# Kernel tuning notes

Hardware: AMD Instinct MI355X
Metric: run time of the kernel (lower is better)

The kernel has to match this reference:

```python
import jax, jax.numpy as jnp
import numpy as np

BITS = 4
MAXQ = (1 << BITS) - 1  # 15
PACK_BITS = 32
GROUP_SIZE = 128


def setup_inputs() -> dict:
    key = jax.random.key(0)
    k1, k2, k3, k4, k5 = jax.random.split(key, 5)
    in_f, out_f, tokens = 4096, 11008, 8192
    pack_factor = PACK_BITS // BITS  # 8
    n_groups = in_f // GROUP_SIZE  # 32
    x = jax.random.normal(k1, (tokens, in_f), dtype=jnp.float32)
    qweight = jax.random.randint(k2, (in_f // pack_factor, out_f), 0, 2147483647, dtype=jnp.int32)
    qzeros = jax.random.randint(k3, (n_groups, out_f // pack_factor), 0, 2147483647, dtype=jnp.int32)
    scales = jax.random.uniform(k4, (n_groups, out_f), dtype=jnp.float32) * 0.01 + 1e-3
    bias = jax.random.normal(k5, (out_f,), dtype=jnp.float32)
    g_idx = (jnp.arange(in_f, dtype=jnp.int32) // GROUP_SIZE).astype(jnp.int32)
    return {"x": x, "qweight": qweight, "qzeros": qzeros, "scales": scales, "bias": bias, "g_idx": g_idx}


def _dequantize(qweight, qzeros, scales, g_idx, in_features):
    # wf = [0, 4, 8, ..., 28]
    shifts = jnp.arange(0, PACK_BITS, BITS, dtype=jnp.int32)
    # unpack zeros: [G, out/8] -> [G, out/8, 8] -> [G, out]
    zeros = (qzeros[:, :, None] >> shifts[None, None, :]) & MAXQ
    zeros = zeros.reshape(scales.shape)
    # unpack weight: [in/8, out] -> [in/8, 8, out] -> [in, out]
    w = (qweight[:, None, :] >> shifts[None, :, None]) & MAXQ
    w = w.reshape(-1, scales.shape[1])[:in_features]
    # dequant: scales[g_idx] * (w - zeros[g_idx])
    return scales[g_idx] * (w - zeros[g_idx]).astype(scales.dtype)


def reference(x, qweight, qzeros, scales, bias, g_idx):
    W = _dequantize(qweight, qzeros, scales, g_idx, x.shape[1])  # [in, out]
    return x @ W + bias
```

## Files before the change

kernel.cpp:

```cpp
#include <hip/hip_runtime.h>
#include <hip/hip_bf16.h>

typedef __attribute__((ext_vector_type(8))) short short8;
typedef __attribute__((ext_vector_type(4))) float f32x4;
typedef __attribute__((ext_vector_type(4))) unsigned int uint4v;

#define BM 256
#define BN 256
#define BK 64

__device__ __forceinline__ void gl_lds16(const __hip_bfloat16* g, __hip_bfloat16* l) {
  __builtin_amdgcn_global_load_lds((const __attribute__((address_space(1))) void*)g,
                                   (__attribute__((address_space(3))) void*)l,
                                   16, 0, 0);
}

__global__ void prep_kernel(const int* __restrict__ qweight,
                            const int* __restrict__ qzeros,
                            const float* __restrict__ scales,
                            __hip_bfloat16* __restrict__ wp,
                            const float* __restrict__ x,
                            __hip_bfloat16* __restrict__ xp,
                            int N, int K, int M, int nDeq) {
  __shared__ __hip_bfloat16 tile[64 * 64];
  const int id = blockIdx.x;
  if (id < nDeq) {
    const int nb = N >> 8;
    const int n = (id % nb) * 256 + threadIdx.x;
    const int kc = id / nb;
    const int g = kc >> 4;
    const float s = scales[(size_t)g * N + n];
    const int zq = qzeros[(size_t)g * (N >> 3) + (n >> 3)];
    const float c = s * (float)((zq >> ((n & 7) * 4)) & 15);
    const int q = qweight[(size_t)kc * N + n];
    __hip_bfloat16 v[8];
#pragma unroll
    for (int j = 0; j < 8; j++)
      v[j] = __float2bfloat16(fmaf(s, (float)((q >> (4 * j)) & 15), -c));
    ((uint4v*)wp)[(size_t)kc * N + n] = *(const uint4v*)v;
  } else {
    const int id2 = id - nDeq;
    const int mb = M >> 6;
    const int m0 = (id2 % mb) * 64, k0 = (id2 / mb) * 64;
    const int t = threadIdx.x;
    const int mr = t >> 2, cq = t & 3;
    const float4* src = (const float4*)(x + (size_t)(m0 + mr) * K + k0 + cq * 16);
    const float4 a = src[0], b = src[1], c = src[2], d = src[3];
    __hip_bfloat16 v[16];
    v[0] = __float2bfloat16(a.x);  v[1] = __float2bfloat16(a.y);
    v[2] = __float2bfloat16(a.z);  v[3] = __float2bfloat16(a.w);
    v[4] = __float2bfloat16(b.x);  v[5] = __float2bfloat16(b.y);
    v[6] = __float2bfloat16(b.z);  v[7] = __float2bfloat16(b.w);
    v[8] = __float2bfloat16(c.x);  v[9] = __float2bfloat16(c.y);
    v[10] = __float2bfloat16(c.z); v[11] = __float2bfloat16(c.w);
    v[12] = __float2bfloat16(d.x); v[13] = __float2bfloat16(d.y);
    v[14] = __float2bfloat16(d.z); v[15] = __float2bfloat16(d.w);
    *(uint4v*)&tile[((cq * 2 + 0) * 64 + mr) * 8] = *(const uint4v*)&v[0];
    *(uint4v*)&tile[((cq * 2 + 1) * 64 + mr) * 8] = *(const uint4v*)&v[8];
    __syncthreads();
#pragma unroll
    for (int j = 0; j < 2; j++) {
      const int s = j * 256 + t;
      const int c8 = s >> 6, m = s & 63;
      ((uint4v*)xp)[(size_t)((k0 >> 3) + c8) * M + m0 + m] = *(const uint4v*)&tile[s * 8];
    }
  }
}

__global__ __launch_bounds__(512, 2) void gemm_kernel(
    const __hip_bfloat16* __restrict__ Xp,
    const __hip_bfloat16* __restrict__ Wp,
    const float* __restrict__ bias,
    float* __restrict__ C, int M, int N, int K) {
  __shared__ __hip_bfloat16 As[2][8 * 256 * 8];
  __shared__ __hip_bfloat16 Bs[2][8 * 256 * 8];
  const int tid = threadIdx.x;
  const int m0 = blockIdx.x * BM;
  const int n0 = blockIdx.y * BN;
  const int wid = tid >> 6, ln = tid & 63;
  const int wmoff = (wid >> 2) * 128;
  const int wnoff = (wid & 3) * 64;
  const int lr = ln & 15, q4 = ln >> 4;

  f32x4 acc[8][4] = {};
  const int NT = K >> 6;

  auto stageA = [&](int t, int hs, int buf) {
#pragma unroll
    for (int i = 0; i < 2; ++i) {
      const int s = i * 512 + tid;
      const int c8 = (hs << 2) + (s >> 8);
      const int row = s & 255;
      gl_lds16(Xp + ((size_t)(t * 8 + c8) * M + m0 + row) * 8,
               &As[buf][(c8 * 256 + row) * 8]);
    }
  };
  auto stageB = [&](int t, int hs, int buf) {
#pragma unroll
    for (int i = 0; i < 2; ++i) {
      const int s = i * 512 + tid;
      const int c8 = (hs << 2) + (s >> 8);
      const int row = s & 255;
      gl_lds16(Wp + ((size_t)(t * 8 + c8) * N + n0 + row) * 8,
               &Bs[buf][(c8 * 256 + row) * 8]);
    }
  };

  stageA(0, 0, 0); stageA(0, 1, 0); stageB(0, 0, 0); stageB(0, 1, 0);
  if (NT > 1) {
    stageA(1, 0, 1); stageB(1, 0, 1); stageA(1, 1, 1);
    asm volatile("s_waitcnt vmcnt(6)" ::: "memory");
  } else {
    asm volatile("s_waitcnt vmcnt(0)" ::: "memory");
  }
  __builtin_amdgcn_s_barrier();

  short8 a[2][4], b0[2][2], b1[2][2];

  for (int t = 0; t < NT; ++t) {
    const int cur = t & 1, nxt = cur ^ 1;
    const __hip_bfloat16* Ac = As[cur];
    const __hip_bfloat16* Bc = Bs[cur];

#pragma unroll
    for (int ks = 0; ks < 2; ++ks) {
#pragma unroll
      for (int mf = 0; mf < 4; ++mf)
        a[ks][mf] = *(const short8*)&Ac[((ks * 4 + q4) * 256 + wmoff + mf * 16 + lr) * 8];
#pragma unroll
      for (int nf = 0; nf < 2; ++nf)
        b0[ks][nf] = *(const short8*)&Bc[((ks * 4 + q4) * 256 + wnoff + nf * 16 + lr) * 8];
    }
    if (t + 1 < NT) stageB(t + 1, 1, nxt);
    __builtin_amdgcn_s_barrier();
    asm volatile("s_waitcnt lgkmcnt(0)" ::: "memory");
    __builtin_amdgcn_s_setprio(1);
#pragma unroll
    for (int mf = 0; mf < 4; ++mf)
#pragma unroll
      for (int nf = 0; nf < 2; ++nf) {
        acc[mf][nf] = __builtin_amdgcn_mfma_f32_16x16x32_bf16(a[0][mf], b0[0][nf], acc[mf][nf], 0, 0, 0);
        acc[mf][nf] = __builtin_amdgcn_mfma_f32_16x16x32_bf16(a[1][mf], b0[1][nf], acc[mf][nf], 0, 0, 0);
      }
    __builtin_amdgcn_s_setprio(0);
    __builtin_amdgcn_s_barrier();

#pragma unroll
    for (int ks = 0; ks < 2; ++ks)
#pragma unroll
      for (int nf = 0; nf < 2; ++nf)
        b1[ks][nf] = *(const short8*)&Bc[((ks * 4 + q4) * 256 + wnoff + 32 + nf * 16 + lr) * 8];
    __builtin_amdgcn_s_barrier();
    asm volatile("s_waitcnt lgkmcnt(0)" ::: "memory");
    __builtin_amdgcn_s_setprio(1);
#pragma unroll
    for (int mf = 0; mf < 4; ++mf)
#pragma unroll
      for (int nf = 0; nf < 2; ++nf) {
        acc[mf][2 + nf] = __builtin_amdgcn_mfma_f32_16x16x32_bf16(a[0][mf], b1[0][nf], acc[mf][2 + nf], 0, 0, 0);
        acc[mf][2 + nf] = __builtin_amdgcn_mfma_f32_16x16x32_bf16(a[1][mf], b1[1][nf], acc[mf][2 + nf], 0, 0, 0);
      }
    __builtin_amdgcn_s_setprio(0);
    __builtin_amdgcn_s_barrier();

#pragma unroll
    for (int ks = 0; ks < 2; ++ks)
#pragma unroll
      for (int mf = 0; mf < 4; ++mf)
        a[ks][mf] = *(const short8*)&Ac[((ks * 4 + q4) * 256 + wmoff + 64 + mf * 16 + lr) * 8];
    if (t + 2 < NT) stageB(t + 2, 0, cur);
    __builtin_amdgcn_s_barrier();
    asm volatile("s_waitcnt lgkmcnt(0)" ::: "memory");
    __builtin_amdgcn_s_setprio(1);
#pragma unroll
    for (int mf = 0; mf < 4; ++mf)
#pragma unroll
      for (int nf = 0; nf < 2; ++nf) {
        acc[4 + mf][2 + nf] = __builtin_amdgcn_mfma_f32_16x16x32_bf16(a[0][mf], b1[0][nf], acc[4 + mf][2 + nf], 0, 0, 0);
        acc[4 + mf][2 + nf] = __builtin_amdgcn_mfma_f32_16x16x32_bf16(a[1][mf], b1[1][nf], acc[4 + mf][2 + nf], 0, 0, 0);
      }
    __builtin_amdgcn_s_setprio(0);
    __builtin_amdgcn_s_barrier();

    if (t + 2 < NT) { stageA(t + 2, 0, cur); stageA(t + 2, 1, cur); }
    if (t == NT - 2) asm volatile("s_waitcnt vmcnt(0)" ::: "memory");
    else             asm volatile("s_waitcnt vmcnt(6)" ::: "memory");
    __builtin_amdgcn_s_barrier();
    __builtin_amdgcn_s_setprio(1);
#pragma unroll
    for (int mf = 0; mf < 4; ++mf)
#pragma unroll
      for (int nf = 0; nf < 2; ++nf) {
        acc[4 + mf][nf] = __builtin_amdgcn_mfma_f32_16x16x32_bf16(a[0][mf], b0[0][nf], acc[4 + mf][nf], 0, 0, 0);
        acc[4 + mf][nf] = __builtin_amdgcn_mfma_f32_16x16x32_bf16(a[1][mf], b0[1][nf], acc[4 + mf][nf], 0, 0, 0);
      }
    __builtin_amdgcn_s_setprio(0);
    __builtin_amdgcn_s_barrier();
  }

  const int cr = m0 + wmoff + q4 * 4;
  const int cc = n0 + wnoff + lr;
#pragma unroll
  for (int nf = 0; nf < 4; ++nf) {
    const float bv = bias[cc + nf * 16];
#pragma unroll
    for (int mf = 0; mf < 8; ++mf) {
#pragma unroll
      for (int r = 0; r < 4; ++r) {
        C[(size_t)(cr + mf * 16 + r) * N + cc + nf * 16] = acc[mf][nf][r] + bv;
      }
    }
  }
}

__global__ void naive_kernel(const float* __restrict__ x, const int* __restrict__ qweight,
                             const int* __restrict__ qzeros, const float* __restrict__ scales,
                             const float* __restrict__ bias, const int* __restrict__ g_idx,
                             float* __restrict__ out, int in_f, int out_f) {
  const int n = blockIdx.x * blockDim.x + threadIdx.x;
  if (n >= out_f) return;
  const int m = blockIdx.y;
  const float* xr = x + (size_t)m * in_f;
  float acc = 0.f;
  for (int kk = 0; kk < (in_f >> 3); kk++) {
    const int q = qweight[(size_t)kk * out_f + n];
    const int g = g_idx[kk * 8];
    const float s = scales[(size_t)g * out_f + n];
    const int z = (qzeros[(size_t)g * (out_f >> 3) + (n >> 3)] >> ((n & 7) * 4)) & 15;
    float part = 0.f;
#pragma unroll
    for (int j = 0; j < 8; j++)
      part += xr[kk * 8 + j] * (float)(((q >> (4 * j)) & 15) - z);
    acc += s * part;
  }
  out[(size_t)m * out_f + n] = acc + bias[n];
}

extern "C" void kernel_launch(void* const* d_in, const int* in_sizes, int n_in,
                              void* d_out, int out_size, void* d_ws, size_t ws_size,
                              hipStream_t stream) {
  const float* x = (const float*)d_in[0];
  const int* qweight = (const int*)d_in[1];
  const int* qzeros = (const int*)d_in[2];
  const float* scales = (const float*)d_in[3];
  const float* bias = (const float*)d_in[4];
  const int* g_idx = (const int*)d_in[5];
  float* out = (float*)d_out;

  const int out_f = in_sizes[4];
  const int in_f = in_sizes[5];
  const int tokens = in_sizes[0] / in_f;

  const size_t need_w = (size_t)in_f * out_f * sizeof(__hip_bfloat16);
  const size_t need_x = (size_t)tokens * in_f * sizeof(__hip_bfloat16);

  if (ws_size >= need_w + need_x && (in_f % 128) == 0 && (out_f % 256) == 0 &&
      (tokens % 256) == 0) {
    __hip_bfloat16* wp = (__hip_bfloat16*)d_ws;
    __hip_bfloat16* xp = (__hip_bfloat16*)((char*)d_ws + need_w);
    const int nDeq = (out_f >> 8) * (in_f >> 3);
    const int nCvt = (tokens >> 6) * (in_f >> 6);
    prep_kernel<<<dim3(nDeq + nCvt), 256, 0, stream>>>(
        qweight, qzeros, scales, wp, x, xp, out_f, in_f, tokens, nDeq);
    gemm_kernel<<<dim3(tokens / BM, out_f / BN), 512, 0, stream>>>(
        xp, wp, bias, out, tokens, out_f, in_f);
  } else {
    naive_kernel<<<dim3((out_f + 255) / 256, tokens), 256, 0, stream>>>(
        x, qweight, qzeros, scales, bias, g_idx, out, in_f, out_f);
  }
}
```

Baseline: 1.222 ms.

## Fuse int4 weight dequantization into GEMM B-tile staging

Measured after the change: 1.675 ms. +37.1%, slower.

```diff
diff --git a/kernel.cpp b/kernel.cpp
--- a/kernel.cpp
+++ b/kernel.cpp
@@ -15,61 +15,39 @@
                                    16, 0, 0);
 }
 
-__global__ void prep_kernel(const int* __restrict__ qweight,
-                            const int* __restrict__ qzeros,
-                            const float* __restrict__ scales,
-                            __hip_bfloat16* __restrict__ wp,
-                            const float* __restrict__ x,
-                            __hip_bfloat16* __restrict__ xp,
-                            int N, int K, int M, int nDeq) {
+__global__ void cvtx_kernel(const float* __restrict__ x,
+                            __hip_bfloat16* __restrict__ xp, int M, int K) {
   __shared__ __hip_bfloat16 tile[64 * 64];
-  const int id = blockIdx.x;
-  if (id < nDeq) {
-    const int nb = N >> 8;
-    const int n = (id % nb) * 256 + threadIdx.x;
-    const int kc = id / nb;
-    const int g = kc >> 4;
-    const float s = scales[(size_t)g * N + n];
-    const int zq = qzeros[(size_t)g * (N >> 3) + (n >> 3)];
-    const float c = s * (float)((zq >> ((n & 7) * 4)) & 15);
-    const int q = qweight[(size_t)kc * N + n];
-    __hip_bfloat16 v[8];
-#pragma unroll
-    for (int j = 0; j < 8; j++)
-      v[j] = __float2bfloat16(fmaf(s, (float)((q >> (4 * j)) & 15), -c));
-    ((uint4v*)wp)[(size_t)kc * N + n] = *(const uint4v*)v;
-  } else {
-    const int id2 = id - nDeq;
-    const int mb = M >> 6;
-    const int m0 = (id2 % mb) * 64, k0 = (id2 / mb) * 64;
-    const int t = threadIdx.x;
-    const int mr = t >> 2, cq = t & 3;
-    const float4* src = (const float4*)(x + (size_t)(m0 + mr) * K + k0 + cq * 16);
-    const float4 a = src[0], b = src[1], c = src[2], d = src[3];
-    __hip_bfloat16 v[16];
-    v[0] = __float2bfloat16(a.x);  v[1] = __float2bfloat16(a.y);
-    v[2] = __float2bfloat16(a.z);  v[3] = __float2bfloat16(a.w);
-    v[4] = __float2bfloat16(b.x);  v[5] = __float2bfloat16(b.y);
-    v[6] = __float2bfloat16(b.z);  v[7] = __float2bfloat16(b.w);
-    v[8] = __float2bfloat16(c.x);  v[9] = __float2bfloat16(c.y);
-    v[10] = __float2bfloat16(c.z); v[11] = __float2bfloat16(c.w);
-    v[12] = __float2bfloat16(d.x); v[13] = __float2bfloat16(d.y);
-    v[14] = __float2bfloat16(d.z); v[15] = __float2bfloat16(d.w);
-    *(uint4v*)&tile[((cq * 2 + 0) * 64 + mr) * 8] = *(const uint4v*)&v[0];
-    *(uint4v*)&tile[((cq * 2 + 1) * 64 + mr) * 8] = *(const uint4v*)&v[8];
-    __syncthreads();
-#pragma unroll
-    for (int j = 0; j < 2; j++) {
-      const int s = j * 256 + t;
-      const int c8 = s >> 6, m = s & 63;
-      ((uint4v*)xp)[(size_t)((k0 >> 3) + c8) * M + m0 + m] = *(const uint4v*)&tile[s * 8];
-    }
+  const int t = threadIdx.x;
+  const int m0 = blockIdx.x * 64, k0 = blockIdx.y * 64;
+  const int mr = t >> 2, cq = t & 3;
+  const float4* src = (const float4*)(x + (size_t)(m0 + mr) * K + k0 + cq * 16);
+  const float4 a = src[0], b = src[1], c = src[2], d = src[3];
+  __hip_bfloat16 v[16];
+  v[0] = __float2bfloat16(a.x);  v[1] = __float2bfloat16(a.y);
+  v[2] = __float2bfloat16(a.z);  v[3] = __float2bfloat16(a.w);
+  v[4] = __float2bfloat16(b.x);  v[5] = __float2bfloat16(b.y);
+  v[6] = __float2bfloat16(b.z);  v[7] = __float2bfloat16(b.w);
+  v[8] = __float2bfloat16(c.x);  v[9] = __float2bfloat16(c.y);
+  v[10] = __float2bfloat16(c.z); v[11] = __float2bfloat16(c.w);
+  v[12] = __float2bfloat16(d.x); v[13] = __float2bfloat16(d.y);
+  v[14] = __float2bfloat16(d.z); v[15] = __float2bfloat16(d.w);
+  *(uint4v*)&tile[((cq * 2 + 0) * 64 + mr) * 8] = *(const uint4v*)&v[0];
+  *(uint4v*)&tile[((cq * 2 + 1) * 64 + mr) * 8] = *(const uint4v*)&v[8];
+  __syncthreads();
+#pragma unroll
+  for (int j = 0; j < 2; j++) {
+    const int s = j * 256 + t;
+    const int c8 = s >> 6, m = s & 63;
+    ((uint4v*)xp)[(size_t)((k0 >> 3) + c8) * M + m0 + m] = *(const uint4v*)&tile[s * 8];
   }
 }
 
 __global__ __launch_bounds__(512, 2) void gemm_kernel(
     const __hip_bfloat16* __restrict__ Xp,
-    const __hip_bfloat16* __restrict__ Wp,
+    const int* __restrict__ qweight,
+    const int* __restrict__ qzeros,
+    const float* __restrict__ scales,
     const float* __restrict__ bias,
     float* __restrict__ C, int M, int N, int K) {
   __shared__ __hip_bfloat16 As[2][8 * 256 * 8];
@@ -82,6 +60,9 @@
   const int wnoff = (wid & 3) * 64;
   const int lr = ln & 15, q4 = ln >> 4;
 
+  const int brow = tid & 255, tb = tid >> 8;
+  const int ngl = n0 + brow;
+
   f32x4 acc[8][4] = {};
   const int NT = K >> 6;
 
@@ -95,27 +76,42 @@
                &As[buf][(c8 * 256 + row) * 8]);
     }
   };
-  auto stageB = [&](int t, int hs, int buf) {
-#pragma unroll
-    for (int i = 0; i < 2; ++i) {
-      const int s = i * 512 + tid;
-      const int c8 = (hs << 2) + (s >> 8);
-      const int row = s & 255;
-      gl_lds16(Wp + ((size_t)(t * 8 + c8) * N + n0 + row) * 8,
-               &Bs[buf][(c8 * 256 + row) * 8]);
-    }
-  };
-
-  stageA(0, 0, 0); stageA(0, 1, 0); stageB(0, 0, 0); stageB(0, 1, 0);
-  if (NT > 1) {
-    stageA(1, 0, 1); stageB(1, 0, 1); stageA(1, 1, 1);
-    asm volatile("s_waitcnt vmcnt(6)" ::: "memory");
-  } else {
-    asm volatile("s_waitcnt vmcnt(0)" ::: "memory");
-  }
+
+  struct BStage { int q0, q1; float s, c; };
+  auto loadB = [&](int t, int hs) -> BStage {
+    BStage r;
+    const int g = t >> 1;
+    r.s = scales[(size_t)g * N + ngl];
+    const int zq = qzeros[(size_t)g * (N >> 3) + (ngl >> 3)];
+    r.c = r.s * (float)((zq >> ((ngl & 7) * 4)) & 15);
+    r.q0 = qweight[(size_t)(t * 8 + (hs << 2) + tb) * N + ngl];
+    r.q1 = qweight[(size_t)(t * 8 + (hs << 2) + tb + 2) * N + ngl];
+    return r;
+  };
+  auto unpack8 = [&](int q, float s, float c, __hip_bfloat16* dst) {
+    __hip_bfloat16 v[8];
+#pragma unroll
+    for (int j = 0; j < 8; j++)
+      v[j] = __float2bfloat16(fmaf(s, (float)((q >> (4 * j)) & 15), -c));
+    *(uint4v*)dst = *(const uint4v*)v;
+  };
+  auto writeB = [&](const BStage& r, int hs, int buf) {
+    unpack8(r.q0, r.s, r.c, &Bs[buf][(((hs << 2) + tb) * 256 + brow) * 8]);
+    unpack8(r.q1, r.s, r.c, &Bs[buf][(((hs << 2) + tb + 2) * 256 + brow) * 8]);
+  };
+
+  stageA(0, 0, 0); stageA(0, 1, 0);
+  BStage b00 = loadB(0, 0);
+  BStage b01 = loadB(0, 1);
+  if (NT > 1) { stageA(1, 0, 1); stageA(1, 1, 1); }
+  writeB(b00, 0, 0);
+  writeB(b01, 1, 0);
+  if (NT > 1) { BStage b10 = loadB(1, 0); writeB(b10, 0, 1); }
+  asm volatile("s_waitcnt vmcnt(0) lgkmcnt(0)" ::: "memory");
   __builtin_amdgcn_s_barrier();
 
   short8 a[2][4], b0[2][2], b1[2][2];
+  BStage bh3{}, bh2{};
 
   for (int t = 0; t < NT; ++t) {
     const int cur = t & 1, nxt = cur ^ 1;
@@ -131,7 +127,7 @@
       for (int nf = 0; nf < 2; ++nf)
         b0[ks][nf] = *(const short8*)&Bc[((ks * 4 + q4) * 256 + wnoff + nf * 16 + lr) * 8];
     }
-    if (t + 1 < NT) stageB(t + 1, 1, nxt);
+    if (t + 1 < NT) bh3 = loadB(t + 1, 1);
     __builtin_amdgcn_s_barrier();
     asm volatile("s_waitcnt lgkmcnt(0)" ::: "memory");
     __builtin_amdgcn_s_setprio(1);
@@ -150,6 +146,7 @@
 #pragma unroll
       for (int nf = 0; nf < 2; ++nf)
         b1[ks][nf] = *(const short8*)&Bc[((ks * 4 + q4) * 256 + wnoff + 32 + nf * 16 + lr) * 8];
+    if (t + 1 < NT) writeB(bh3, 1, nxt);
     __builtin_amdgcn_s_barrier();
     asm volatile("s_waitcnt lgkmcnt(0)" ::: "memory");
     __builtin_amdgcn_s_setprio(1);
@@ -168,7 +165,7 @@
 #pragma unroll
       for (int mf = 0; mf < 4; ++mf)
         a[ks][mf] = *(const short8*)&Ac[((ks * 4 + q4) * 256 + wmoff + 64 + mf * 16 + lr) * 8];
-    if (t + 2 < NT) stageB(t + 2, 0, cur);
+    if (t + 2 < NT) bh2 = loadB(t + 2, 0);
     __builtin_amdgcn_s_barrier();
     asm volatile("s_waitcnt lgkmcnt(0)" ::: "memory");
     __builtin_amdgcn_s_setprio(1);
@@ -182,10 +179,14 @@
     __builtin_amdgcn_s_setprio(0);
     __builtin_amdgcn_s_barrier();
 
-    if (t + 2 < NT) { stageA(t + 2, 0, cur); stageA(t + 2, 1, cur); }
+    if (t + 2 < NT) {
+      stageA(t + 2, 0, cur); stageA(t + 2, 1, cur);
+      writeB(bh2, 0, cur);
+    }
     if (t == NT - 2) asm volatile("s_waitcnt vmcnt(0)" ::: "memory");
-    else             asm volatile("s_waitcnt vmcnt(6)" ::: "memory");
-    __builtin_amdgcn_s_barrier();
+    else             asm volatile("s_waitcnt vmcnt(4)" ::: "memory");
+    __builtin_amdgcn_s_barrier();
+    asm volatile("s_waitcnt lgkmcnt(0)" ::: "memory");
     __builtin_amdgcn_s_setprio(1);
 #pragma unroll
     for (int mf = 0; mf < 4; ++mf)
@@ -251,19 +252,14 @@
   const int in_f = in_sizes[5];
   const int tokens = in_sizes[0] / in_f;
 
-  const size_t need_w = (size_t)in_f * out_f * sizeof(__hip_bfloat16);
   const size_t need_x = (size_t)tokens * in_f * sizeof(__hip_bfloat16);
 
-  if (ws_size >= need_w + need_x && (in_f % 128) == 0 && (out_f % 256) == 0 &&
+  if (ws_size >= need_x && (in_f % 128) == 0 && (out_f % 256) == 0 &&
       (tokens % 256) == 0) {
-    __hip_bfloat16* wp = (__hip_bfloat16*)d_ws;
-    __hip_bfloat16* xp = (__hip_bfloat16*)((char*)d_ws + need_w);
-    const int nDeq = (out_f >> 8) * (in_f >> 3);
-    const int nCvt = (tokens >> 6) * (in_f >> 6);
-    prep_kernel<<<dim3(nDeq + nCvt), 256, 0, stream>>>(
-        qweight, qzeros, scales, wp, x, xp, out_f, in_f, tokens, nDeq);
+    __hip_bfloat16* xp = (__hip_bfloat16*)d_ws;
+    cvtx_kernel<<<dim3(tokens / 64, in_f / 64), 256, 0, stream>>>(x, xp, tokens, in_f);
     gemm_kernel<<<dim3(tokens / BM, out_f / BN), 512, 0, stream>>>(
-        xp, wp, bias, out, tokens, out_f, in_f);
+        xp, qweight, qzeros, scales, bias, out, tokens, out_f, in_f);
   } else {
     naive_kernel<<<dim3((out_f + 255) / 256, tokens), 256, 0, stream>>>(
         x, qweight, qzeros, scales, bias, g_idx, out, in_f, out_f);
```
